# Optimization experiments

Measured on AMD Instinct MI355X. Metric: run time of the kernel, lower is better.

## Reference

```python
import jax, jax.numpy as jnp
import numpy as np

NUM_HEADS = 8
HEAD_DIM = 16  # hidden_size 128 / 8 heads
SCALE = float(np.sqrt(HEAD_DIM))


def setup_inputs() -> dict:
    key = jax.random.key(0)
    k1, k2, k3, k4 = jax.random.split(key, 4)
    B, N, H = 1, 50000, 128
    E = 800000
    q = jax.random.normal(k1, (B, N, H), dtype=jnp.float32)
    k = jax.random.normal(k2, (B, N, H), dtype=jnp.float32)
    v = jax.random.normal(k3, (B, N, H), dtype=jnp.float32)
    edge_index = jax.random.randint(k4, (2, E), 0, N, dtype=jnp.int64)
    return {"q": q, "k": k, "v": v, "edge_index": edge_index}


def reference(q, k, v, edge_index):
    B, N, H = q.shape
    total = B * N
    qh = q.reshape(total, NUM_HEADS, HEAD_DIM)
    kh = k.reshape(total, NUM_HEADS, HEAD_DIM)
    vh = v.reshape(total, NUM_HEADS, HEAD_DIM)
    src_idx = edge_index[0]
    dst_idx = edge_index[1]
    src = kh[src_idx]          # [E, heads, d]
    dest = qh[dst_idx]         # [E, heads, d]
    # per-edge scaled dot score, clamped then exponentiated
    score = jnp.sum(src * dest / SCALE, axis=-1, keepdims=True)  # [E, heads, 1]
    score = jnp.exp(jnp.clip(score, -5.0, 5.0))
    msg = vh[src_idx] * score  # [E, heads, d]
    wV = jax.ops.segment_sum(msg, dst_idx, num_segments=total)    # [total, heads, d]
    Z = jax.ops.segment_sum(score, dst_idx, num_segments=total)   # [total, heads, 1]
    x = wV / (Z + 1e-6)
    return x.reshape(B, N, NUM_HEADS * HEAD_DIM)
```

## Files before the change

### kernel.cpp

```cpp
#include <hip/hip_runtime.h>

#define HID 128
#define NPB 4
#define CHUNK 16384
#define CSHIFT 14
#define MAXW 25088

typedef unsigned short u16;
typedef unsigned int u32;

__device__ __forceinline__ float bf2f(u16 u) { return __uint_as_float(((u32)u) << 16); }
__device__ __forceinline__ u16 f2bf(float f) {
    u32 x = __float_as_uint(f);
    return (u16)((x + 0x7FFF + ((x >> 16) & 1)) >> 16);
}

__global__ void pack_kernel(const float* __restrict__ k, const float* __restrict__ v,
                            u16* __restrict__ kv, int N) {
    int g = blockIdx.x * 256 + threadIdx.x;
    int node = g >> 6, l = g & 63;
    if (node >= N) return;
    float2 kk = ((const float2*)(k + (long long)node * HID))[l];
    float2 vv = ((const float2*)(v + (long long)node * HID))[l];
    ushort4 o;
    o.x = f2bf(kk.x * 0.25f);
    o.y = f2bf(kk.y * 0.25f);
    o.z = f2bf(vv.x);
    o.w = f2bf(vv.y);
    ((ushort4*)(kv + (long long)node * 256))[l] = o;
}

__global__ __launch_bounds__(1024) void hist_kernel(const int* __restrict__ ei,
        u32* __restrict__ Hp, u16* __restrict__ lrank, int E, int W) {
    __shared__ u32 hcnt[MAXW];
    int c = blockIdx.x;
    for (int j = threadIdx.x; j < W; j += 1024) hcnt[j] = 0;
    __syncthreads();
    int beg = c << CSHIFT;
    int end = min(E, beg + CHUNK);
    for (int i = beg + (int)threadIdx.x; i < end; i += 1024) {
        int d = ei[E + i];
        u32 sh = (u32)(d & 1) << 4;
        u32 old = atomicAdd(&hcnt[d >> 1], 1u << sh);
        lrank[i] = (u16)((old >> sh) & 0xFFFFu);
    }
    __syncthreads();
    for (int j = threadIdx.x; j < W; j += 1024) Hp[(size_t)c * W + j] = hcnt[j];
}

__global__ void scan_node_kernel(u32* __restrict__ Hp, u32* __restrict__ t,
                                 int W, int NB, int N) {
    int j = blockIdx.x * blockDim.x + threadIdx.x;
    if (j >= W) return;
    u32 lo = 0, hi = 0;
    for (int c = 0; c < NB; c++) {
        size_t idx = (size_t)c * W + j;
        u32 w = Hp[idx];
        Hp[idx] = lo | (hi << 16);
        lo += w & 0xFFFFu;
        hi += w >> 16;
    }
    int n0 = 2 * j, n1 = 2 * j + 1;
    if (n0 < N) t[n0] = lo;
    if (n1 < N) t[n1] = hi;
}

__global__ void scanA_kernel(const u32* __restrict__ counts, int* __restrict__ offsets,
                             int* __restrict__ partials, int M) {
    __shared__ int sdata[256];
    int tid = threadIdx.x;
    int base = blockIdx.x * 2048 + tid * 8;
    int v[8];
    int tsum = 0;
    for (int j = 0; j < 8; j++) {
        int idx = base + j;
        v[j] = (idx < M) ? (int)counts[idx] : 0;
        tsum += v[j];
    }
    sdata[tid] = tsum;
    __syncthreads();
    for (int off = 1; off < 256; off <<= 1) {
        int x = sdata[tid];
        int y = (tid >= off) ? sdata[tid - off] : 0;
        __syncthreads();
        sdata[tid] = x + y;
        __syncthreads();
    }
    int excl = sdata[tid] - tsum;
    for (int j = 0; j < 8; j++) {
        int idx = base + j;
        if (idx < M) offsets[idx] = excl;
        excl += v[j];
    }
    if (tid == 255) partials[blockIdx.x] = sdata[255];
}

__global__ void scanC_kernel(int* __restrict__ offsets, const int* __restrict__ partials,
                             int M, int E, int nbA) {
    __shared__ int sp[256];
    int tid = threadIdx.x;
    if (tid == 0) {
        int run = 0;
        for (int i = 0; i < nbA; i++) { sp[i] = run; run += partials[i]; }
    }
    __syncthreads();
    int idx = blockIdx.x * blockDim.x + tid;
    if (idx < M) offsets[idx] += sp[idx >> 11];
    if (idx == 0) offsets[M] = E;
}

__global__ void scatter_kernel(const int* __restrict__ ei, const u32* __restrict__ Hp,
                               const u16* __restrict__ lrank, const int* __restrict__ offsets,
                               u16* __restrict__ srcs, int E, int W) {
    int e = blockIdx.x * blockDim.x + threadIdx.x;
    if (e >= E) return;
    int c = e >> CSHIFT;
    int d = ei[E + e];
    u32 sh = (u32)(d & 1) << 4;
    u32 b = (Hp[(size_t)c * W + (d >> 1)] >> sh) & 0xFFFFu;
    int pos = offsets[d] + (int)b + (int)lrank[e];
    srcs[pos] = (u16)ei[e];
}

__global__ __launch_bounds__(256) void reduce_packed(
        const float* __restrict__ q, const u16* __restrict__ kv,
        const int* __restrict__ offsets, const u16* __restrict__ srcs,
        float* __restrict__ out, int N) {
    int node = blockIdx.x * NPB + (threadIdx.x >> 6);
    if (node >= N) return;
    int l = threadIdx.x & 63;

    float2 qv = ((const float2*)(q + (long long)node * HID))[l];
    const char* kvb = (const char*)kv;
    u32 lane8 = (u32)l << 3;
    float accx = 0.0f, accy = 0.0f, z = 0.0f;

    int beg = offsets[node];
    int end = offsets[node + 1];
    int i = beg;

#define LOADKV(srcv) (*(const ushort4*)(kvb + (((u32)(srcv) << 9) + lane8)))

    for (; i + 8 <= end; i += 8) {
        u32 s0 = srcs[i + 0], s1 = srcs[i + 1], s2 = srcs[i + 2], s3 = srcs[i + 3];
        u32 s4 = srcs[i + 4], s5 = srcs[i + 5], s6 = srcs[i + 6], s7 = srcs[i + 7];
        ushort4 a0 = LOADKV(s0);
        ushort4 a1 = LOADKV(s1);
        ushort4 a2 = LOADKV(s2);
        ushort4 a3 = LOADKV(s3);
        ushort4 a4 = LOADKV(s4);
        ushort4 a5 = LOADKV(s5);
        ushort4 a6 = LOADKV(s6);
        ushort4 a7 = LOADKV(s7);

        float p0 = bf2f(a0.x) * qv.x + bf2f(a0.y) * qv.y;
        float p1 = bf2f(a1.x) * qv.x + bf2f(a1.y) * qv.y;
        float p2 = bf2f(a2.x) * qv.x + bf2f(a2.y) * qv.y;
        float p3 = bf2f(a3.x) * qv.x + bf2f(a3.y) * qv.y;
        float p4 = bf2f(a4.x) * qv.x + bf2f(a4.y) * qv.y;
        float p5 = bf2f(a5.x) * qv.x + bf2f(a5.y) * qv.y;
        float p6 = bf2f(a6.x) * qv.x + bf2f(a6.y) * qv.y;
        float p7 = bf2f(a7.x) * qv.x + bf2f(a7.y) * qv.y;

        p0 += __shfl_xor(p0, 1); p1 += __shfl_xor(p1, 1);
        p2 += __shfl_xor(p2, 1); p3 += __shfl_xor(p3, 1);
        p4 += __shfl_xor(p4, 1); p5 += __shfl_xor(p5, 1);
        p6 += __shfl_xor(p6, 1); p7 += __shfl_xor(p7, 1);
        p0 += __shfl_xor(p0, 2); p1 += __shfl_xor(p1, 2);
        p2 += __shfl_xor(p2, 2); p3 += __shfl_xor(p3, 2);
        p4 += __shfl_xor(p4, 2); p5 += __shfl_xor(p5, 2);
        p6 += __shfl_xor(p6, 2); p7 += __shfl_xor(p7, 2);
        p0 += __shfl_xor(p0, 4); p1 += __shfl_xor(p1, 4);
        p2 += __shfl_xor(p2, 4); p3 += __shfl_xor(p3, 4);
        p4 += __shfl_xor(p4, 4); p5 += __shfl_xor(p5, 4);
        p6 += __shfl_xor(p6, 4); p7 += __shfl_xor(p7, 4);

        float c0 = __expf(fminf(fmaxf(p0, -5.0f), 5.0f));
        float c1 = __expf(fminf(fmaxf(p1, -5.0f), 5.0f));
        float c2 = __expf(fminf(fmaxf(p2, -5.0f), 5.0f));
        float c3 = __expf(fminf(fmaxf(p3, -5.0f), 5.0f));
        float c4 = __expf(fminf(fmaxf(p4, -5.0f), 5.0f));
        float c5 = __expf(fminf(fmaxf(p5, -5.0f), 5.0f));
        float c6 = __expf(fminf(fmaxf(p6, -5.0f), 5.0f));
        float c7 = __expf(fminf(fmaxf(p7, -5.0f), 5.0f));

        accx += bf2f(a0.z) * c0 + bf2f(a1.z) * c1 + bf2f(a2.z) * c2 + bf2f(a3.z) * c3
              + bf2f(a4.z) * c4 + bf2f(a5.z) * c5 + bf2f(a6.z) * c6 + bf2f(a7.z) * c7;
        accy += bf2f(a0.w) * c0 + bf2f(a1.w) * c1 + bf2f(a2.w) * c2 + bf2f(a3.w) * c3
              + bf2f(a4.w) * c4 + bf2f(a5.w) * c5 + bf2f(a6.w) * c6 + bf2f(a7.w) * c7;
        z += c0 + c1 + c2 + c3 + c4 + c5 + c6 + c7;
    }
    for (; i < end; i++) {
        u32 s = srcs[i];
        ushort4 a = LOADKV(s);
        float p = bf2f(a.x) * qv.x + bf2f(a.y) * qv.y;
        p += __shfl_xor(p, 1);
        p += __shfl_xor(p, 2);
        p += __shfl_xor(p, 4);
        float c = __expf(fminf(fmaxf(p, -5.0f), 5.0f));
        accx += bf2f(a.z) * c;
        accy += bf2f(a.w) * c;
        z += c;
    }
#undef LOADKV
    float inv = 1.0f / (z + 1e-6f);
    ((float2*)(out + (long long)node * HID))[l] = make_float2(accx * inv, accy * inv);
}


__global__ void count_kernel(const int* __restrict__ ei, int* __restrict__ counts,
                             int* __restrict__ pos, int E) {
    int e = blockIdx.x * blockDim.x + threadIdx.x;
    if (e < E) pos[e] = atomicAdd(&counts[ei[E + e]], 1);
}

__global__ void fill_kernel(const int* __restrict__ ei, const int* __restrict__ offsets,
                            const int* __restrict__ pos, int* __restrict__ srcs, int E) {
    int e = blockIdx.x * blockDim.x + threadIdx.x;
    if (e < E) srcs[offsets[ei[E + e]] + pos[e]] = ei[e];
}

__global__ __launch_bounds__(256) void reduce_f32(
        const float* __restrict__ q, const float* __restrict__ k,
        const float* __restrict__ v, const int* __restrict__ offsets,
        const int* __restrict__ srcs, float* __restrict__ out, int N) {
    int node = blockIdx.x * NPB + (threadIdx.x >> 6);
    if (node >= N) return;
    int l = threadIdx.x & 63;
    float2 qv = ((const float2*)(q + (long long)node * HID))[l];
    float accx = 0.0f, accy = 0.0f, z = 0.0f;
    int beg = offsets[node], end = offsets[node + 1];
    for (int i = beg; i < end; i++) {
        int s = srcs[i];
        float2 kk = ((const float2*)(k + (long long)s * HID))[l];
        float2 vv = ((const float2*)(v + (long long)s * HID))[l];
        float p = (kk.x * qv.x + kk.y * qv.y) * 0.25f;
        p += __shfl_xor(p, 1);
        p += __shfl_xor(p, 2);
        p += __shfl_xor(p, 4);
        float c = __expf(fminf(fmaxf(p, -5.0f), 5.0f));
        accx += vv.x * c; accy += vv.y * c; z += c;
    }
    float inv = 1.0f / (z + 1e-6f);
    ((float2*)(out + (long long)node * HID))[l] = make_float2(accx * inv, accy * inv);
}

extern "C" void kernel_launch(void* const* d_in, const int* in_sizes, int n_in,
                              void* d_out, int out_size, void* d_ws, size_t ws_size,
                              hipStream_t stream) {
    const float* q = (const float*)d_in[0];
    const float* k = (const float*)d_in[1];
    const float* v = (const float*)d_in[2];
    const int* ei = (const int*)d_in[3];
    float* out = (float*)d_out;

    int E = in_sizes[3] / 2;
    int N = in_sizes[0] / HID;

    int block = 256;
    int eblocks = (E + block - 1) / block;
    int nbA = (N + 2047) / 2048;
    int nblocksN = (N + 255) / 256;
    int rgrid = (N + NPB - 1) / NPB;

    int W = (N + 1) / 2;
    int NB = (E + CHUNK - 1) >> CSHIFT;

    size_t kv_bytes = (size_t)N * 256 * sizeof(u16);
    size_t need = kv_bytes + ((size_t)NB * W + N + N + 1 + 256) * 4
                + 2 * ((size_t)E + 8) * 2 + 64;

    bool primary = (W <= MAXW) && (nbA <= 256) && (ws_size >= need);

    if (primary) {
        u16* kv = (u16*)d_ws;
        u32* Hp = (u32*)((char*)d_ws + kv_bytes);
        u32* t = Hp + (size_t)NB * W;
        int* offsets = (int*)(t + N);
        int* partials = offsets + N + 1;
        u16* lrank = (u16*)(partials + 256);
        u16* srcs = lrank + ((E + 8) & ~1);

        pack_kernel<<<(N * 64 + 255) / 256, 256, 0, stream>>>(k, v, kv, N);
        hist_kernel<<<NB, 1024, 0, stream>>>(ei, Hp, lrank, E, W);
        scan_node_kernel<<<(W + 255) / 256, 256, 0, stream>>>(Hp, t, W, NB, N);
        scanA_kernel<<<nbA, 256, 0, stream>>>(t, offsets, partials, N);
        scanC_kernel<<<nblocksN, 256, 0, stream>>>(offsets, partials, N, E, nbA);
        scatter_kernel<<<eblocks, 256, 0, stream>>>(ei, Hp, lrank, offsets, srcs, E, W);
        reduce_packed<<<rgrid, 256, 0, stream>>>(q, kv, offsets, srcs, out, N);
    } else {
        int* counts = (int*)d_ws;
        int* offsets = counts + N;
        int* partials = offsets + N + 1;
        int* pos = partials + 256;
        int* srcs = pos + E;

        hipMemsetAsync(counts, 0, (size_t)N * sizeof(int), stream);
        count_kernel<<<eblocks, 256, 0, stream>>>(ei, counts, pos, E);
        scanA_kernel<<<nbA, 256, 0, stream>>>((const u32*)counts, offsets, partials, N);
        scanC_kernel<<<nblocksN, 256, 0, stream>>>(offsets, partials, N, E, nbA);
        fill_kernel<<<eblocks, 256, 0, stream>>>(ei, offsets, pos, srcs, E);
        reduce_f32<<<rgrid, 256, 0, stream>>>(q, k, v, offsets, srcs, out, N);
    }
}
```

Measured before the change: 126.2 us.

## Split each wavefront into two half-waves processing separate edges with 16-byte loads

The packed reduce kernel now has each 64-lane wavefront handle two edges at once. Each 32-lane half loads 16 bytes per lane (4 K and 4 V bf16 values) instead of 8 bytes, and the two halves' partial sums are combined with a cross-half shuffle at the end. This halves the per-edge shuffle depth and loop iterations and widens memory transactions, aimed at a latency-bound gather. Block size drops to 128 threads with 2 nodes per block. The cost is extra final shuffles and idle lanes during the output store.

Result: faster. 122.3 us (-3.1%).

```diff
diff --git a/kernel.cpp b/kernel.cpp
--- a/kernel.cpp
+++ b/kernel.cpp
@@ -1,7 +1,6 @@
 #include <hip/hip_runtime.h>
 
 #define HID 128
-#define NPB 4
 #define CHUNK 16384
 #define CSHIFT 14
 #define MAXW 25088
@@ -10,6 +9,8 @@
 typedef unsigned int u32;
 
 __device__ __forceinline__ float bf2f(u16 u) { return __uint_as_float(((u32)u) << 16); }
+__device__ __forceinline__ float lof(u32 w) { return __uint_as_float(w << 16); }
+__device__ __forceinline__ float hif(u32 w) { return __uint_as_float(w & 0xFFFF0000u); }
 __device__ __forceinline__ u16 f2bf(float f) {
     u32 x = __float_as_uint(f);
     return (u16)((x + 0x7FFF + ((x >> 16) & 1)) >> 16);
@@ -122,89 +123,88 @@
     srcs[pos] = (u16)ei[e];
 }
 
-__global__ __launch_bounds__(256) void reduce_packed(
+__global__ __launch_bounds__(128) void reduce_packed(
         const float* __restrict__ q, const u16* __restrict__ kv,
         const int* __restrict__ offsets, const u16* __restrict__ srcs,
         float* __restrict__ out, int N) {
-    int node = blockIdx.x * NPB + (threadIdx.x >> 6);
+    int node = blockIdx.x * 2 + (threadIdx.x >> 6);
     if (node >= N) return;
     int l = threadIdx.x & 63;
-
-    float2 qv = ((const float2*)(q + (long long)node * HID))[l];
+    int m = l & 31;
+    int half = l >> 5;
+
+    float4 qv = ((const float4*)(q + (long long)node * HID))[m];
     const char* kvb = (const char*)kv;
-    u32 lane8 = (u32)l << 3;
-    float accx = 0.0f, accy = 0.0f, z = 0.0f;
+    u32 laneoff = (u32)m << 4;
+    float4 acc = make_float4(0.0f, 0.0f, 0.0f, 0.0f);
+    float z = 0.0f;
 
     int beg = offsets[node];
     int end = offsets[node + 1];
     int i = beg;
 
-#define LOADKV(srcv) (*(const ushort4*)(kvb + (((u32)(srcv) << 9) + lane8)))
+#define GLOAD(s_) (*(const uint4*)(kvb + (((u32)(s_) << 9) + laneoff)))
 
     for (; i + 8 <= end; i += 8) {
-        u32 s0 = srcs[i + 0], s1 = srcs[i + 1], s2 = srcs[i + 2], s3 = srcs[i + 3];
-        u32 s4 = srcs[i + 4], s5 = srcs[i + 5], s6 = srcs[i + 6], s7 = srcs[i + 7];
-        ushort4 a0 = LOADKV(s0);
-        ushort4 a1 = LOADKV(s1);
-        ushort4 a2 = LOADKV(s2);
-        ushort4 a3 = LOADKV(s3);
-        ushort4 a4 = LOADKV(s4);
-        ushort4 a5 = LOADKV(s5);
-        ushort4 a6 = LOADKV(s6);
-        ushort4 a7 = LOADKV(s7);
-
-        float p0 = bf2f(a0.x) * qv.x + bf2f(a0.y) * qv.y;
-        float p1 = bf2f(a1.x) * qv.x + bf2f(a1.y) * qv.y;
-        float p2 = bf2f(a2.x) * qv.x + bf2f(a2.y) * qv.y;
-        float p3 = bf2f(a3.x) * qv.x + bf2f(a3.y) * qv.y;
-        float p4 = bf2f(a4.x) * qv.x + bf2f(a4.y) * qv.y;
-        float p5 = bf2f(a5.x) * qv.x + bf2f(a5.y) * qv.y;
-        float p6 = bf2f(a6.x) * qv.x + bf2f(a6.y) * qv.y;
-        float p7 = bf2f(a7.x) * qv.x + bf2f(a7.y) * qv.y;
+        u32 sA0 = srcs[i + 0], sB0 = srcs[i + 1];
+        u32 sA1 = srcs[i + 2], sB1 = srcs[i + 3];
+        u32 sA2 = srcs[i + 4], sB2 = srcs[i + 5];
+        u32 sA3 = srcs[i + 6], sB3 = srcs[i + 7];
+        uint4 a0 = GLOAD(half ? sB0 : sA0);
+        uint4 a1 = GLOAD(half ? sB1 : sA1);
+        uint4 a2 = GLOAD(half ? sB2 : sA2);
+        uint4 a3 = GLOAD(half ? sB3 : sA3);
+
+        float p0 = lof(a0.x) * qv.x + hif(a0.x) * qv.y + lof(a0.z) * qv.z + hif(a0.z) * qv.w;
+        float p1 = lof(a1.x) * qv.x + hif(a1.x) * qv.y + lof(a1.z) * qv.z + hif(a1.z) * qv.w;
+        float p2 = lof(a2.x) * qv.x + hif(a2.x) * qv.y + lof(a2.z) * qv.z + hif(a2.z) * qv.w;
+        float p3 = lof(a3.x) * qv.x + hif(a3.x) * qv.y + lof(a3.z) * qv.z + hif(a3.z) * qv.w;
 
         p0 += __shfl_xor(p0, 1); p1 += __shfl_xor(p1, 1);
         p2 += __shfl_xor(p2, 1); p3 += __shfl_xor(p3, 1);
-        p4 += __shfl_xor(p4, 1); p5 += __shfl_xor(p5, 1);
-        p6 += __shfl_xor(p6, 1); p7 += __shfl_xor(p7, 1);
         p0 += __shfl_xor(p0, 2); p1 += __shfl_xor(p1, 2);
         p2 += __shfl_xor(p2, 2); p3 += __shfl_xor(p3, 2);
-        p4 += __shfl_xor(p4, 2); p5 += __shfl_xor(p5, 2);
-        p6 += __shfl_xor(p6, 2); p7 += __shfl_xor(p7, 2);
-        p0 += __shfl_xor(p0, 4); p1 += __shfl_xor(p1, 4);
-        p2 += __shfl_xor(p2, 4); p3 += __shfl_xor(p3, 4);
-        p4 += __shfl_xor(p4, 4); p5 += __shfl_xor(p5, 4);
-        p6 += __shfl_xor(p6, 4); p7 += __shfl_xor(p7, 4);
 
         float c0 = __expf(fminf(fmaxf(p0, -5.0f), 5.0f));
         float c1 = __expf(fminf(fmaxf(p1, -5.0f), 5.0f));
         float c2 = __expf(fminf(fmaxf(p2, -5.0f), 5.0f));
         float c3 = __expf(fminf(fmaxf(p3, -5.0f), 5.0f));
-        float c4 = __expf(fminf(fmaxf(p4, -5.0f), 5.0f));
-        float c5 = __expf(fminf(fmaxf(p5, -5.0f), 5.0f));
-        float c6 = __expf(fminf(fmaxf(p6, -5.0f), 5.0f));
-        float c7 = __expf(fminf(fmaxf(p7, -5.0f), 5.0f));
-
-        accx += bf2f(a0.z) * c0 + bf2f(a1.z) * c1 + bf2f(a2.z) * c2 + bf2f(a3.z) * c3
-              + bf2f(a4.z) * c4 + bf2f(a5.z) * c5 + bf2f(a6.z) * c6 + bf2f(a7.z) * c7;
-        accy += bf2f(a0.w) * c0 + bf2f(a1.w) * c1 + bf2f(a2.w) * c2 + bf2f(a3.w) * c3
-              + bf2f(a4.w) * c4 + bf2f(a5.w) * c5 + bf2f(a6.w) * c6 + bf2f(a7.w) * c7;
-        z += c0 + c1 + c2 + c3 + c4 + c5 + c6 + c7;
-    }
-    for (; i < end; i++) {
-        u32 s = srcs[i];
-        ushort4 a = LOADKV(s);
-        float p = bf2f(a.x) * qv.x + bf2f(a.y) * qv.y;
+
+        acc.x += lof(a0.y) * c0 + lof(a1.y) * c1 + lof(a2.y) * c2 + lof(a3.y) * c3;
+        acc.y += hif(a0.y) * c0 + hif(a1.y) * c1 + hif(a2.y) * c2 + hif(a3.y) * c3;
+        acc.z += lof(a0.w) * c0 + lof(a1.w) * c1 + lof(a2.w) * c2 + lof(a3.w) * c3;
+        acc.w += hif(a0.w) * c0 + hif(a1.w) * c1 + hif(a2.w) * c2 + hif(a3.w) * c3;
+        z += c0 + c1 + c2 + c3;
+    }
+    for (; i < end; i += 2) {
+        int idx = i + half;
+        bool ok = idx < end;
+        u32 s = srcs[ok ? idx : i];
+        uint4 a = GLOAD(s);
+        float p = lof(a.x) * qv.x + hif(a.x) * qv.y + lof(a.z) * qv.z + hif(a.z) * qv.w;
         p += __shfl_xor(p, 1);
         p += __shfl_xor(p, 2);
-        p += __shfl_xor(p, 4);
         float c = __expf(fminf(fmaxf(p, -5.0f), 5.0f));
-        accx += bf2f(a.z) * c;
-        accy += bf2f(a.w) * c;
+        c = ok ? c : 0.0f;
+        acc.x += lof(a.y) * c;
+        acc.y += hif(a.y) * c;
+        acc.z += lof(a.w) * c;
+        acc.w += hif(a.w) * c;
         z += c;
     }
-#undef LOADKV
-    float inv = 1.0f / (z + 1e-6f);
-    ((float2*)(out + (long long)node * HID))[l] = make_float2(accx * inv, accy * inv);
+#undef GLOAD
+
+    acc.x += __shfl_xor(acc.x, 32);
+    acc.y += __shfl_xor(acc.y, 32);
+    acc.z += __shfl_xor(acc.z, 32);
+    acc.w += __shfl_xor(acc.w, 32);
+    z     += __shfl_xor(z, 32);
+
+    if (half == 0) {
+        float inv = 1.0f / (z + 1e-6f);
+        ((float4*)(out + (long long)node * HID))[m] =
+            make_float4(acc.x * inv, acc.y * inv, acc.z * inv, acc.w * inv);
+    }
 }
 
 
@@ -224,7 +224,7 @@
         const float* __restrict__ q, const float* __restrict__ k,
         const float* __restrict__ v, const int* __restrict__ offsets,
         const int* __restrict__ srcs, float* __restrict__ out, int N) {
-    int node = blockIdx.x * NPB + (threadIdx.x >> 6);
+    int node = blockIdx.x * 4 + (threadIdx.x >> 6);
     if (node >= N) return;
     int l = threadIdx.x & 63;
     float2 qv = ((const float2*)(q + (long long)node * HID))[l];
@@ -261,7 +261,6 @@
     int eblocks = (E + block - 1) / block;
     int nbA = (N + 2047) / 2048;
     int nblocksN = (N + 255) / 256;
-    int rgrid = (N + NPB - 1) / NPB;
 
     int W = (N + 1) / 2;
     int NB = (E + CHUNK - 1) >> CSHIFT;
@@ -287,7 +286,8 @@
         scanA_kernel<<<nbA, 256, 0, stream>>>(t, offsets, partials, N);
         scanC_kernel<<<nblocksN, 256, 0, stream>>>(offsets, partials, N, E, nbA);
         scatter_kernel<<<eblocks, 256, 0, stream>>>(ei, Hp, lrank, offsets, srcs, E, W);
-        reduce_packed<<<rgrid, 256, 0, stream>>>(q, kv, offsets, srcs, out, N);
+        int rgrid = (N + 1) / 2;
+        reduce_packed<<<rgrid, 128, 0, stream>>>(q, kv, offsets, srcs, out, N);
     } else {
         int* counts = (int*)d_ws;
         int* offsets = counts + N;
@@ -300,6 +300,7 @@
         scanA_kernel<<<nbA, 256, 0, stream>>>((const u32*)counts, offsets, partials, N);
         scanC_kernel<<<nblocksN, 256, 0, stream>>>(offsets, partials, N, E, nbA);
         fill_kernel<<<eblocks, 256, 0, stream>>>(ei, offsets, pos, srcs, E);
+        int rgrid = (N + 3) / 4;
         reduce_f32<<<rgrid, 256, 0, stream>>>(q, k, v, offsets, srcs, out, N);
     }
 }
```
